# Performance work log

Measured on AMD Instinct MI355X. Metric: run time of the kernel, lower is better.

## Reference

```python
import jax, jax.numpy as jnp
import numpy as np

LN_EPS = 1e-5


def _ln(x, g, b):
    m = jnp.mean(x, axis=-1, keepdims=True)
    v = jnp.mean((x - m) ** 2, axis=-1, keepdims=True)
    return (x - m) / jnp.sqrt(v + LN_EPS) * g + b


def setup_inputs() -> dict:
    key = jax.random.key(0)
    ks = jax.random.split(key, 8)
    B, N, S, D, T = 16, 64, 2048, 1024, 768

    def xavier(k, shape):
        fan_in, fan_out = shape
        lim = (6.0 / (fan_in + fan_out)) ** 0.5
        return jax.random.uniform(k, shape, minval=-lim, maxval=lim, dtype=jnp.float32)

    return {
        "prev_states": jax.random.normal(ks[0], (B, N, D), dtype=jnp.float32),
        "input_tokens": jax.random.normal(ks[1], (B, S, T), dtype=jnp.float32),
        # input_projection (token_dim -> state_dim)
        "W_proj": xavier(ks[2], (T, D)),
        "b_proj": jnp.zeros((D,), jnp.float32),
        # three LayerNorms
        "g_state": jnp.ones((D,), jnp.float32), "beta_state": jnp.zeros((D,), jnp.float32),
        "g_input": jnp.ones((D,), jnp.float32), "beta_input": jnp.zeros((D,), jnp.float32),
        "g_out": jnp.ones((D,), jnp.float32), "beta_out": jnp.zeros((D,), jnp.float32),
        # GRU gates (2D -> D); update-gate bias initialized to -1 as in the module
        "W_u": xavier(ks[3], (2 * D, D)), "b_u": jnp.full((D,), -1.0, jnp.float32),
        "W_r": xavier(ks[4], (2 * D, D)), "b_r": jnp.zeros((D,), jnp.float32),
        "W_n": xavier(ks[5], (2 * D, D)), "b_n": jnp.zeros((D,), jnp.float32),
    }


def reference(prev_states, input_tokens, W_proj, b_proj,
              g_state, beta_state, g_input, beta_input, g_out, beta_out,
              W_u, b_u, W_r, b_r, W_n, b_n):
    D = prev_states.shape[-1]
    # project tokens to state dim: (B,S,D)
    tok = input_tokens @ W_proj + b_proj
    # attention routing (routing_weights=None path)
    scores = jnp.einsum('bnd,bsd->bns', prev_states, tok) / jnp.sqrt(jnp.float32(D))
    attn = jax.nn.softmax(scores, axis=-1)
    routed = jnp.einsum('bns,bsd->bnd', attn, tok)  # (B,N,D)
    # GRU-style gated update, vectorized over the num_states axis
    ps_n = _ln(prev_states, g_state, beta_state)
    in_n = _ln(routed, g_input, beta_input)
    concat = jnp.concatenate([ps_n, in_n], axis=-1)  # (B,N,2D)
    u = jax.nn.sigmoid(concat @ W_u + b_u)
    r = jax.nn.sigmoid(concat @ W_r + b_r)
    reset_in = jnp.concatenate([r * ps_n, in_n], axis=-1)
    cand = jnp.tanh(reset_in @ W_n + b_n)  # dropout is identity in eval
    new_state = (1.0 - u) * prev_states + u * cand
    return _ln(new_state, g_out, beta_out)
```

## Files before the change

### kernel.cpp

```cpp
#include <hip/hip_runtime.h>
#include <stdint.h>

typedef __attribute__((ext_vector_type(4))) float floatx4;
typedef __attribute__((ext_vector_type(8))) short shortx8;

#define LN_EPS 1e-5f

__device__ __forceinline__ unsigned short f2b(float f) {
  unsigned u = __builtin_bit_cast(unsigned, f);
  u = (u + 0x7FFFu + ((u >> 16) & 1u)) >> 16;
  return (unsigned short)u;
}
__device__ __forceinline__ float b2f(unsigned short h) {
  return __builtin_bit_cast(float, (unsigned)h << 16);
}

__device__ __forceinline__ void g2l16(const unsigned short* g, unsigned short* l) {
  __builtin_amdgcn_global_load_lds(
      (const __attribute__((address_space(1))) unsigned int*)g,
      (__attribute__((address_space(3))) unsigned int*)l, 16, 0, 0);
}

__device__ __forceinline__ float wave_sum(float v) {
#pragma unroll
  for (int o = 32; o; o >>= 1) v += __shfl_down(v, o, 64);
  return v;
}
__device__ __forceinline__ float block_sum(float v, float* s) {
  v = wave_sum(v);
  __syncthreads();
  if ((threadIdx.x & 63) == 0) s[threadIdx.x >> 6] = v;
  __syncthreads();
  return s[0] + s[1] + s[2] + s[3];
}

__global__ __launch_bounds__(256) void k_prep(
    const float* __restrict__ prev, unsigned short* __restrict__ psb,
    const float* __restrict__ wp, unsigned short* __restrict__ wpb,
    const float* __restrict__ Wu, const float* __restrict__ Wr,
    const float* __restrict__ Wn,
    unsigned short* __restrict__ Wtur, unsigned short* __restrict__ Wtn,
    unsigned short* __restrict__ Wtp, float* __restrict__ rs) {
  __shared__ float tile[32][33];
  const int bid = blockIdx.x;
  if (bid < 896) {
    if (bid == 0) {
      floatx4 z = {0.f, 0.f, 0.f, 0.f};
      *(floatx4*)(rs + threadIdx.x * 4) = z;
    }
    const float* src;
    unsigned short* dst;
    long i;
    if (bid < 512) { src = prev; dst = psb; i = ((long)bid * 256 + threadIdx.x) * 8; }
    else { src = wp; dst = wpb; i = ((long)(bid - 512) * 256 + threadIdx.x) * 8; }
    floatx4 v0 = *(const floatx4*)(src + i);
    floatx4 v1 = *(const floatx4*)(src + i + 4);
    unsigned short t8[8];
#pragma unroll
    for (int j = 0; j < 4; j++) { t8[j] = f2b(v0[j]); t8[4 + j] = f2b(v1[j]); }
    *(uint4*)(dst + i) = *(uint4*)t8;
    return;
  }
  int t = bid - 896;
  const float* in;
  unsigned short* out;
  int K, kx, ny;
  if (t < 6144) {
    const int which = t >> 11;
    const int t2 = t & 2047;
    kx = t2 & 63;
    ny = t2 >> 6;
    K = 2048;
    in = which == 0 ? Wu : (which == 1 ? Wr : Wn);
    out = which == 0 ? Wtur : (which == 1 ? Wtur + 1024 * 2048 : Wtn);
  } else {
    const int t2 = t - 6144;
    kx = t2 % 24;
    ny = t2 / 24;
    K = 768;
    in = wp;
    out = Wtp;
  }
  const int N = 1024;
  const int k0 = kx * 32, n0 = ny * 32;
  const int tx = threadIdx.x & 31, ty = threadIdx.x >> 5;
#pragma unroll
  for (int i = 0; i < 32; i += 8)
    tile[ty + i][tx] = in[(long)(k0 + ty + i) * N + n0 + tx];
  __syncthreads();
#pragma unroll
  for (int i = 0; i < 32; i += 8)
    out[(long)(n0 + ty + i) * K + k0 + tx] = f2b(tile[tx][ty + i]);
}

__global__ __launch_bounds__(256) void k_gemm64(
    const unsigned short* __restrict__ A, int lda,
    const unsigned short* __restrict__ Bt, int ldb,
    int K, long sCk,
    const float* __restrict__ bias, const float* __restrict__ bias2,
    int mode,
    void* __restrict__ out, int ldc,
    unsigned short* __restrict__ out2,
    const unsigned short* __restrict__ aux_psn) {
  __shared__ unsigned short As[2][64 * 64];
  __shared__ unsigned short Bs[2][64 * 64];
  const int tid = threadIdx.x;
  const int wave = tid >> 6, lane = tid & 63;
  const int kc = blockIdx.z;
  const long koff = (long)kc * K;
  const int flat = blockIdx.x + blockIdx.y * gridDim.x;
  const int q = (gridDim.x * gridDim.y) >> 3;
  const int swz = (flat & 7) * q + (flat >> 3);
  const int m0 = (swz % gridDim.x) * 64;
  const int n0 = (swz / gridDim.x) * 64;
  const int wm = wave & 1, wn = wave >> 1;
  const int l16 = lane & 15, quad = lane >> 4;
  const int srow8 = lane >> 3;
  const int c8 = ((lane & 7) ^ srow8) * 8;

  const unsigned short* gA[2];
  const unsigned short* gB[2];
  int lOff[2];
#pragma unroll
  for (int j = 0; j < 2; j++) {
    const int rb = wave * 16 + j * 8;
    gA[j] = A + (long)(m0 + rb + srow8) * lda + c8 + koff;
    gB[j] = Bt + (long)(n0 + rb + srow8) * ldb + c8 + koff;
    lOff[j] = rb * 64;
  }
  int offA[2][2], offB[2][2];
#pragma unroll
  for (int ks = 0; ks < 2; ks++)
#pragma unroll
    for (int i = 0; i < 2; i++) {
      int r = wm * 32 + i * 16 + l16;
      offA[ks][i] = r * 64 + (((ks * 4 + quad) ^ (r & 7)) * 8);
      r = wn * 32 + i * 16 + l16;
      offB[ks][i] = r * 64 + (((ks * 4 + quad) ^ (r & 7)) * 8);
    }

  floatx4 acc[2][2] = {};

#pragma unroll
  for (int j = 0; j < 2; j++) {
    g2l16(gA[j], &As[0][lOff[j]]);
    g2l16(gB[j], &Bs[0][lOff[j]]);
  }
  __syncthreads();

  const int nt = K >> 6;
  for (int t = 0; t < nt; t++) {
    const int cur = t & 1;
    if (t + 1 < nt) {
      const int kn = (t + 1) << 6;
#pragma unroll
      for (int j = 0; j < 2; j++) {
        g2l16(gA[j] + kn, &As[cur ^ 1][lOff[j]]);
        g2l16(gB[j] + kn, &Bs[cur ^ 1][lOff[j]]);
      }
    }
#pragma unroll
    for (int ks = 0; ks < 2; ks++) {
      shortx8 af[2], bf[2];
#pragma unroll
      for (int i = 0; i < 2; i++) af[i] = *(const shortx8*)&As[cur][offA[ks][i]];
#pragma unroll
      for (int j = 0; j < 2; j++) bf[j] = *(const shortx8*)&Bs[cur][offB[ks][j]];
#pragma unroll
      for (int i = 0; i < 2; i++)
#pragma unroll
        for (int j = 0; j < 2; j++)
          acc[i][j] = __builtin_amdgcn_mfma_f32_16x16x32_bf16(af[i], bf[j], acc[i][j], 0, 0, 0);
    }
    __syncthreads();
  }

#pragma unroll
  for (int i = 0; i < 2; i++)
#pragma unroll
    for (int j = 0; j < 2; j++) {
      const int rbase = m0 + wm * 32 + i * 16 + quad * 4;
      const int c = n0 + wn * 32 + j * 16 + l16;
      float bval = 0.0f;
      if (bias) bval = (mode == 5 && c >= 1024) ? bias2[c - 1024] : bias[c];
#pragma unroll
      for (int r = 0; r < 4; r++) {
        const int row = rbase + r;
        float v = acc[i][j][r] + bval;
        if (mode == 1) {
          out2[(long)row * ldc + c] = f2b(v);
        } else if (mode == 7) {
          ((float*)out)[(long)kc * sCk + (long)row * ldc + c] = v;
        } else {
          if (c < 1024) {
            ((float*)out)[(long)row * 1024 + c] = 1.0f / (1.0f + expf(-v));
          } else {
            const int cc = c - 1024;
            float rr = 1.0f / (1.0f + expf(-v));
            out2[(long)row * 2048 + cc] = f2b(rr * b2f(aux_psn[(long)row * 2048 + cc]));
          }
        }
      }
    }
}

__global__ __launch_bounds__(256) void k_gemm64_af32(
    const float* __restrict__ P0, int lda,
    const unsigned short* __restrict__ Bt, int ldb,
    int K,
    const float* __restrict__ bp, const float* __restrict__ rowsum,
    float* __restrict__ out, int ldc) {
  __shared__ unsigned short As[2][64 * 64];
  __shared__ unsigned short Bs[2][64 * 64];
  const int tid = threadIdx.x;
  const int wave = tid >> 6, lane = tid & 63;
  const int flat = blockIdx.x + blockIdx.y * gridDim.x;
  const int q = (gridDim.x * gridDim.y) >> 3;
  const int swz = (flat & 7) * q + (flat >> 3);
  const int m0 = (swz % gridDim.x) * 64;
  const int n0 = (swz / gridDim.x) * 64;
  const int wm = wave & 1, wn = wave >> 1;
  const int l16 = lane & 15, quad = lane >> 4;
  const int srow8 = lane >> 3;
  const int c8 = ((lane & 7) ^ srow8) * 8;

  const float* gAf[2];
  const unsigned short* gB[2];
  int lOff[2];
#pragma unroll
  for (int j = 0; j < 2; j++) {
    const int rb = wave * 16 + j * 8;
    gAf[j] = P0 + (long)(m0 + rb + srow8) * lda + c8;
    gB[j] = Bt + (long)(n0 + rb + srow8) * ldb + c8;
    lOff[j] = rb * 64;
  }
  int offA[2][2], offB[2][2];
#pragma unroll
  for (int ks = 0; ks < 2; ks++)
#pragma unroll
    for (int i = 0; i < 2; i++) {
      int r = wm * 32 + i * 16 + l16;
      offA[ks][i] = r * 64 + (((ks * 4 + quad) ^ (r & 7)) * 8);
      r = wn * 32 + i * 16 + l16;
      offB[ks][i] = r * 64 + (((ks * 4 + quad) ^ (r & 7)) * 8);
    }

  floatx4 acc[2][2] = {};

#pragma unroll
  for (int j = 0; j < 2; j++) {
    g2l16(gB[j], &Bs[0][lOff[j]]);
    floatx4 a0 = *(const floatx4*)(gAf[j]);
    floatx4 a1 = *(const floatx4*)(gAf[j] + 4);
    floatx4 b0 = *(const floatx4*)(gAf[j] + 786432);
    floatx4 b1 = *(const floatx4*)(gAf[j] + 786432 + 4);
    unsigned short t8[8];
#pragma unroll
    for (int i = 0; i < 4; i++) { t8[i] = f2b(a0[i] + b0[i]); t8[4 + i] = f2b(a1[i] + b1[i]); }
    *(uint4*)&As[0][lOff[j] + lane * 8] = *(uint4*)t8;
  }
  __syncthreads();

  const int nt = K >> 6;
  for (int t = 0; t < nt; t++) {
    const int cur = t & 1;
    floatx4 a0[2], a1[2], p0[2], p1[2];
    if (t + 1 < nt) {
      const int kn = (t + 1) << 6;
#pragma unroll
      for (int j = 0; j < 2; j++) {
        g2l16(gB[j] + kn, &Bs[cur ^ 1][lOff[j]]);
        a0[j] = *(const floatx4*)(gAf[j] + kn);
        a1[j] = *(const floatx4*)(gAf[j] + kn + 4);
        p0[j] = *(const floatx4*)(gAf[j] + kn + 786432);
        p1[j] = *(const floatx4*)(gAf[j] + kn + 786432 + 4);
      }
    }
#pragma unroll
    for (int ks = 0; ks < 2; ks++) {
      shortx8 af[2], bf[2];
#pragma unroll
      for (int i = 0; i < 2; i++) af[i] = *(const shortx8*)&As[cur][offA[ks][i]];
#pragma unroll
      for (int j = 0; j < 2; j++) bf[j] = *(const shortx8*)&Bs[cur][offB[ks][j]];
#pragma unroll
      for (int i = 0; i < 2; i++)
#pragma unroll
        for (int j = 0; j < 2; j++)
          acc[i][j] = __builtin_amdgcn_mfma_f32_16x16x32_bf16(af[i], bf[j], acc[i][j], 0, 0, 0);
    }
    if (t + 1 < nt) {
#pragma unroll
      for (int j = 0; j < 2; j++) {
        unsigned short t8[8];
#pragma unroll
        for (int i = 0; i < 4; i++) {
          t8[i] = f2b(a0[j][i] + p0[j][i]);
          t8[4 + i] = f2b(a1[j][i] + p1[j][i]);
        }
        *(uint4*)&As[cur ^ 1][lOff[j] + lane * 8] = *(uint4*)t8;
      }
    }
    __syncthreads();
  }

#pragma unroll
  for (int i = 0; i < 2; i++)
#pragma unroll
    for (int j = 0; j < 2; j++) {
      const int rbase = m0 + wm * 32 + i * 16 + quad * 4;
      const int c = n0 + wn * 32 + j * 16 + l16;
#pragma unroll
      for (int r = 0; r < 4; r++) {
        const int row = rbase + r;
        out[(long)row * ldc + c] = acc[i][j][r] + rowsum[row] * bp[c];
      }
    }
}

__global__ __launch_bounds__(256) void k_scores(
    const unsigned short* __restrict__ A, long sAb, int lda,
    const float* __restrict__ toksf,
    int K, float scale,
    unsigned short* __restrict__ out2, int ldc, long sCb,
    float* __restrict__ rs) {
  __shared__ unsigned short As[2][64 * 64];
  __shared__ unsigned short Bs[2][64 * 64];
  const int tid = threadIdx.x;
  const int wave = tid >> 6, lane = tid & 63;
  const int b = blockIdx.z;
  const int m0 = 0, n0 = blockIdx.y * 64;
  const int wm = wave & 1, wn = wave >> 1;
  const int l16 = lane & 15, quad = lane >> 4;
  const int srow8 = lane >> 3;
  const int c8 = ((lane & 7) ^ srow8) * 8;
  const unsigned short* Ab = A + (long)b * sAb;

  const unsigned short* gA[2];
  const float* gBf[2];
  int lOff[2];
#pragma unroll
  for (int j = 0; j < 2; j++) {
    const int rb = wave * 16 + j * 8;
    gA[j] = Ab + (long)(m0 + rb + srow8) * lda + c8;
    gBf[j] = toksf + (long)b * 1572864 + (long)(n0 + rb + srow8) * 768 + c8;
    lOff[j] = rb * 64;
  }
  int offA[2][2], offB[2][2];
#pragma unroll
  for (int ks = 0; ks < 2; ks++)
#pragma unroll
    for (int i = 0; i < 2; i++) {
      int r = wm * 32 + i * 16 + l16;
      offA[ks][i] = r * 64 + (((ks * 4 + quad) ^ (r & 7)) * 8);
      r = wn * 32 + i * 16 + l16;
      offB[ks][i] = r * 64 + (((ks * 4 + quad) ^ (r & 7)) * 8);
    }

  floatx4 acc[2][2] = {};

#pragma unroll
  for (int j = 0; j < 2; j++) {
    g2l16(gA[j], &As[0][lOff[j]]);
    floatx4 v0 = *(const floatx4*)(gBf[j]);
    floatx4 v1 = *(const floatx4*)(gBf[j] + 4);
    unsigned short t8[8];
#pragma unroll
    for (int i = 0; i < 4; i++) { t8[i] = f2b(v0[i]); t8[4 + i] = f2b(v1[i]); }
    *(uint4*)&Bs[0][lOff[j] + lane * 8] = *(uint4*)t8;
  }
  __syncthreads();

  const int nt = K >> 6;
  for (int t = 0; t < nt; t++) {
    const int cur = t & 1;
    floatx4 w0[2], w1[2];
    if (t + 1 < nt) {
      const int kn = (t + 1) << 6;
#pragma unroll
      for (int j = 0; j < 2; j++) {
        g2l16(gA[j] + kn, &As[cur ^ 1][lOff[j]]);
        w0[j] = *(const floatx4*)(gBf[j] + kn);
        w1[j] = *(const floatx4*)(gBf[j] + kn + 4);
      }
    }
#pragma unroll
    for (int ks = 0; ks < 2; ks++) {
      shortx8 af[2], bf[2];
#pragma unroll
      for (int i = 0; i < 2; i++) af[i] = *(const shortx8*)&As[cur][offA[ks][i]];
#pragma unroll
      for (int j = 0; j < 2; j++) bf[j] = *(const shortx8*)&Bs[cur][offB[ks][j]];
#pragma unroll
      for (int i = 0; i < 2; i++)
#pragma unroll
        for (int j = 0; j < 2; j++)
          acc[i][j] = __builtin_amdgcn_mfma_f32_16x16x32_bf16(af[i], bf[j], acc[i][j], 0, 0, 0);
    }
    if (t + 1 < nt) {
#pragma unroll
      for (int j = 0; j < 2; j++) {
        unsigned short t8[8];
#pragma unroll
        for (int i = 0; i < 4; i++) { t8[i] = f2b(w0[j][i]); t8[4 + i] = f2b(w1[j][i]); }
        *(uint4*)&Bs[cur ^ 1][lOff[j] + lane * 8] = *(uint4*)t8;
      }
    }
    __syncthreads();
  }

#pragma unroll
  for (int i = 0; i < 2; i++) {
    float psum[4] = {0.f, 0.f, 0.f, 0.f};
#pragma unroll
    for (int j = 0; j < 2; j++) {
      const int rbase = m0 + wm * 32 + i * 16 + quad * 4;
      const int c = n0 + wn * 32 + j * 16 + l16;
#pragma unroll
      for (int r = 0; r < 4; r++) {
        const float e = expf(acc[i][j][r] * scale);
        out2[(long)b * sCb + (long)(rbase + r) * ldc + c] = f2b(e);
        psum[r] += e;
      }
    }
#pragma unroll
    for (int r = 0; r < 4; r++) {
      float s = psum[r];
      s += __shfl_xor(s, 1, 64);
      s += __shfl_xor(s, 2, 64);
      s += __shfl_xor(s, 4, 64);
      s += __shfl_xor(s, 8, 64);
      if (l16 == 0)
        atomicAdd(rs + (long)b * 64 + m0 + wm * 32 + i * 16 + quad * 4 + r, s);
    }
  }
}

__global__ __launch_bounds__(256) void k_routed_mfma(
    const unsigned short* __restrict__ attnb,
    const float* __restrict__ tokf,
    float* __restrict__ parts) {
  __shared__ unsigned short As[64 * 40];
  __shared__ unsigned short Bs[32 * 66];
  const int kc = blockIdx.x, nt = blockIdx.y, b = blockIdx.z;
  const int tid = threadIdx.x;
  const int wave = tid >> 6, lane = tid & 63;
  const int wm = wave & 1, wn = wave >> 1;
  const int l16 = lane & 15, quad = lane >> 4;
  const int n0 = nt * 64;
  const long abase = (long)b * 131072 + (long)kc * 1024;
  const long tbase = ((long)b * 2048 + (long)kc * 1024) * 768;
  const int srow = tid >> 2, skc = (tid & 3) * 8;
  const int bk = tid >> 3, bd = (tid & 7) * 8;

  floatx4 acc[2][2] = {};

  uint4 pa = *(const uint4*)(attnb + abase + (long)srow * 2048 + skc);
  floatx4 f0 = *(const floatx4*)(tokf + tbase + (long)bk * 768 + n0 + bd);
  floatx4 f1 = *(const floatx4*)(tokf + tbase + (long)bk * 768 + n0 + bd + 4);

  for (int k0 = 0; k0 < 1024; k0 += 32) {
    *(uint4*)&As[srow * 40 + skc] = pa;
    {
      unsigned short t8[8];
#pragma unroll
      for (int i = 0; i < 4; i++) { t8[i] = f2b(f0[i]); t8[4 + i] = f2b(f1[i]); }
      unsigned short* dst = &Bs[bk * 66 + bd];
#pragma unroll
      for (int w2 = 0; w2 < 4; w2++) *(unsigned*)(dst + w2 * 2) = ((unsigned*)t8)[w2];
    }
    if (k0 + 32 < 1024) {
      pa = *(const uint4*)(attnb + abase + (long)srow * 2048 + (k0 + 32) + skc);
      f0 = *(const floatx4*)(tokf + tbase + (long)(k0 + 32 + bk) * 768 + n0 + bd);
      f1 = *(const floatx4*)(tokf + tbase + (long)(k0 + 32 + bk) * 768 + n0 + bd + 4);
    }
    asm volatile("s_waitcnt lgkmcnt(0)" ::: "memory");
    __builtin_amdgcn_s_barrier();
    __builtin_amdgcn_sched_barrier(0);

    shortx8 a0 = *(const shortx8*)&As[(wm * 32 + 0  + l16) * 40 + quad * 8];
    shortx8 a1 = *(const shortx8*)&As[(wm * 32 + 16 + l16) * 40 + quad * 8];
    shortx8 b0, b1;
#pragma unroll
    for (int j = 0; j < 8; j++) {
      b0[j] = *(const short*)&Bs[(quad * 8 + j) * 66 + wn * 32 + l16];
      b1[j] = *(const short*)&Bs[(quad * 8 + j) * 66 + wn * 32 + 16 + l16];
    }
    acc[0][0] = __builtin_amdgcn_mfma_f32_16x16x32_bf16(a0, b0, acc[0][0], 0, 0, 0);
    acc[0][1] = __builtin_amdgcn_mfma_f32_16x16x32_bf16(a0, b1, acc[0][1], 0, 0, 0);
    acc[1][0] = __builtin_amdgcn_mfma_f32_16x16x32_bf16(a1, b0, acc[1][0], 0, 0, 0);
    acc[1][1] = __builtin_amdgcn_mfma_f32_16x16x32_bf16(a1, b1, acc[1][1], 0, 0, 0);
    __builtin_amdgcn_s_barrier();
  }

#pragma unroll
  for (int im = 0; im < 2; im++)
#pragma unroll
    for (int in_ = 0; in_ < 2; in_++) {
      const int rbase = wm * 32 + im * 16 + quad * 4;
      const int c = n0 + wn * 32 + in_ * 16 + l16;
#pragma unroll
      for (int r = 0; r < 4; r++)
        parts[(long)kc * 786432 + ((long)b * 64 + rbase + r) * 768 + c] =
            acc[im][in_][r];
    }
}

__global__ __launch_bounds__(256) void k_ln2(
    const float* __restrict__ prev, const float* __restrict__ routed,
    const float* __restrict__ g_st, const float* __restrict__ be_st,
    const float* __restrict__ g_in, const float* __restrict__ be_in,
    unsigned short* __restrict__ conc, unsigned short* __restrict__ candA) {
  __shared__ float scr[4];
  const long r = blockIdx.x & 1023;
  const bool second = blockIdx.x >= 1024;
  const int t = threadIdx.x;
  floatx4 v;
  const float *g, *be;
  if (!second) {
    v = *(const floatx4*)(prev + r * 1024 + t * 4);
    g = g_st; be = be_st;
  } else {
    v = *(const floatx4*)(routed + r * 1024 + t * 4);
    g = g_in; be = be_in;
  }
  float s1 = v[0] + v[1] + v[2] + v[3];
  float s2 = v[0] * v[0] + v[1] * v[1] + v[2] * v[2] + v[3] * v[3];
  s1 = block_sum(s1, scr);
  s2 = block_sum(s2, scr);
  const float mean = s1 * (1.0f / 1024.0f);
  const float var = s2 * (1.0f / 1024.0f) - mean * mean;
  const float rstd = rsqrtf(var + LN_EPS);
#pragma unroll
  for (int i = 0; i < 4; i++) {
    const int d = t * 4 + i;
    const float y = (v[i] - mean) * rstd * g[d] + be[d];
    const unsigned short h = f2b(y);
    if (!second) {
      conc[r * 2048 + d] = h;
    } else {
      conc[r * 2048 + 1024 + d] = h;
      candA[r * 2048 + 1024 + d] = h;
    }
  }
}

__global__ __launch_bounds__(256) void k_gate_epi(
    const float* __restrict__ gparts,
    const float* __restrict__ bu, const float* __restrict__ br,
    const unsigned short* __restrict__ conc,
    float* __restrict__ ubuf, unsigned short* __restrict__ candA) {
  const int row = blockIdx.x >> 1;
  const int half = blockIdx.x & 1;
  const int t = threadIdx.x;
  const long base = (long)row * 2048 + half * 1024 + t * 4;
  floatx4 p0 = *(const floatx4*)(gparts + base);
  floatx4 p1 = *(const floatx4*)(gparts + 2097152 + base);
  const float* bias = half ? br : bu;
  floatx4 bv = *(const floatx4*)(bias + t * 4);
  if (!half) {
    floatx4 o;
#pragma unroll
    for (int i = 0; i < 4; i++)
      o[i] = 1.0f / (1.0f + expf(-(p0[i] + p1[i] + bv[i])));
    *(floatx4*)(ubuf + (long)row * 1024 + t * 4) = o;
  } else {
    unsigned short t4[4];
#pragma unroll
    for (int i = 0; i < 4; i++) {
      float rr = 1.0f / (1.0f + expf(-(p0[i] + p1[i] + bv[i])));
      t4[i] = f2b(rr * b2f(conc[(long)row * 2048 + t * 4 + i]));
    }
    *(uint2*)(candA + (long)row * 2048 + t * 4) = *(uint2*)t4;
  }
}

__global__ __launch_bounds__(256) void k_ln_out(
    const float* __restrict__ cparts,
    const float* __restrict__ ubuf, const float* __restrict__ prev,
    const float* __restrict__ bn,
    const float* __restrict__ g, const float* __restrict__ be,
    float* __restrict__ out) {
  __shared__ float scr[4];
  const long r = blockIdx.x;
  const int t = threadIdx.x;
  floatx4 p0 = *(const floatx4*)(cparts + r * 1024 + t * 4);
  floatx4 p1 = *(const floatx4*)(cparts + 1048576 + r * 1024 + t * 4);
  floatx4 uu = *(const floatx4*)(ubuf + r * 1024 + t * 4);
  floatx4 pv = *(const floatx4*)(prev + r * 1024 + t * 4);
  floatx4 bv = *(const floatx4*)(bn + t * 4);
  floatx4 v;
#pragma unroll
  for (int i = 0; i < 4; i++) {
    const float cand = tanhf(p0[i] + p1[i] + bv[i]);
    v[i] = (1.0f - uu[i]) * pv[i] + uu[i] * cand;
  }
  float s1 = v[0] + v[1] + v[2] + v[3];
  float s2 = v[0] * v[0] + v[1] * v[1] + v[2] * v[2] + v[3] * v[3];
  s1 = block_sum(s1, scr);
  s2 = block_sum(s2, scr);
  const float mean = s1 * (1.0f / 1024.0f);
  const float var = s2 * (1.0f / 1024.0f) - mean * mean;
  const float rstd = rsqrtf(var + LN_EPS);
  floatx4 o;
#pragma unroll
  for (int i = 0; i < 4; i++) {
    const int d = t * 4 + i;
    o[i] = (v[i] - mean) * rstd * g[d] + be[d];
  }
  *(floatx4*)(out + r * 1024 + t * 4) = o;
}

extern "C" void kernel_launch(void* const* d_in, const int* in_sizes, int n_in,
                              void* d_out, int out_size, void* d_ws, size_t ws_size,
                              hipStream_t stream) {
  (void)in_sizes; (void)n_in; (void)out_size; (void)ws_size;
  const float* prev  = (const float*)d_in[0];
  const float* toks  = (const float*)d_in[1];
  const float* Wp    = (const float*)d_in[2];
  const float* bp    = (const float*)d_in[3];
  const float* g_st  = (const float*)d_in[4];
  const float* be_st = (const float*)d_in[5];
  const float* g_in  = (const float*)d_in[6];
  const float* be_in = (const float*)d_in[7];
  const float* g_o   = (const float*)d_in[8];
  const float* be_o  = (const float*)d_in[9];
  const float* Wu    = (const float*)d_in[10];
  const float* bu    = (const float*)d_in[11];
  const float* Wr    = (const float*)d_in[12];
  const float* br    = (const float*)d_in[13];
  const float* Wn    = (const float*)d_in[14];
  const float* bn    = (const float*)d_in[15];
  float* out = (float*)d_out;

  char* ws = (char*)d_ws;
  unsigned short* psb   = (unsigned short*)ws; ws += 2097152;
  unsigned short* Wpb   = (unsigned short*)ws; ws += 1572864;
  unsigned short* Wtp   = (unsigned short*)ws; ws += 1572864;
  unsigned short* pwb   = (unsigned short*)ws; ws += 1572864;
  unsigned short* attnb = (unsigned short*)ws; ws += 4194304;
  float*          rowsum= (float*)ws;          ws += 4096;
  float*          parts = (float*)ws;          ws += 6291456;
  float*          routed= (float*)ws;          ws += 4194304;
  unsigned short* conc  = (unsigned short*)ws; ws += 4194304;
  unsigned short* candA = (unsigned short*)ws; ws += 4194304;
  float*          ubuf  = (float*)ws;          ws += 4194304;
  unsigned short* Wtur  = (unsigned short*)ws; ws += 8388608;
  unsigned short* Wtn   = (unsigned short*)ws; ws += 4194304;
  float*          gparts= (float*)ws;          ws += 16777216;
  float*          cparts= (float*)ws;          ws += 8388608;

  const dim3 blk(256);

  k_prep<<<dim3(7808), blk, 0, stream>>>(prev, psb, Wp, Wpb,
                                         Wu, Wr, Wn, Wtur, Wtn, Wtp, rowsum);
  k_gemm64<<<dim3(16, 12, 1), blk, 0, stream>>>(
      psb, 1024, Wpb, 1024, 1024, 0L,
      nullptr, nullptr, 1,
      nullptr, 768, pwb, nullptr);
  k_scores<<<dim3(1, 32, 16), blk, 0, stream>>>(
      pwb, 49152L, 768, toks, 768, 0.03125f,
      attnb, 2048, 131072L, rowsum);
  k_routed_mfma<<<dim3(2, 12, 16), blk, 0, stream>>>(attnb, toks, parts);
  k_gemm64_af32<<<dim3(16, 16), blk, 0, stream>>>(
      parts, 768, Wtp, 768, 768, bp, rowsum, routed, 1024);
  k_ln2<<<dim3(2048), blk, 0, stream>>>(prev, routed, g_st, be_st, g_in, be_in,
                                        conc, candA);
  k_gemm64<<<dim3(16, 32, 2), blk, 0, stream>>>(
      conc, 2048, Wtur, 2048, 1024, 2097152L,
      nullptr, nullptr, 7,
      (void*)gparts, 2048, nullptr, nullptr);
  k_gate_epi<<<dim3(2048), blk, 0, stream>>>(gparts, bu, br, conc, ubuf, candA);
  k_gemm64<<<dim3(16, 16, 2), blk, 0, stream>>>(
      candA, 2048, Wtn, 2048, 1024, 1048576L,
      nullptr, nullptr, 7,
      (void*)cparts, 1024, nullptr, nullptr);
  k_ln_out<<<dim3(1024), blk, 0, stream>>>(cparts, ubuf, prev, bn, g_o, be_o, out);
}
```

Baseline: 305.5 us.

## Fuse fp32-to-bf16 conversion into prev×Wp GEMM inside prep kernel; fold state LN into proj GEMM

```diff
diff --git a/kernel.cpp b/kernel.cpp
--- a/kernel.cpp
+++ b/kernel.cpp
@@ -34,34 +34,128 @@
   return s[0] + s[1] + s[2] + s[3];
 }
 
-__global__ __launch_bounds__(256) void k_prep(
-    const float* __restrict__ prev, unsigned short* __restrict__ psb,
-    const float* __restrict__ wp, unsigned short* __restrict__ wpb,
+__global__ __launch_bounds__(256) void k_prep_pw(
+    const float* __restrict__ prev, const float* __restrict__ wp,
     const float* __restrict__ Wu, const float* __restrict__ Wr,
     const float* __restrict__ Wn,
     unsigned short* __restrict__ Wtur, unsigned short* __restrict__ Wtn,
-    unsigned short* __restrict__ Wtp, float* __restrict__ rs) {
-  __shared__ float tile[32][33];
+    unsigned short* __restrict__ Wtp, unsigned short* __restrict__ pwb,
+    float* __restrict__ rs) {
+  __shared__ unsigned short As[2][64 * 64];
+  __shared__ unsigned short Bs[2][64 * 64];
   const int bid = blockIdx.x;
-  if (bid < 896) {
-    if (bid == 0) {
-      floatx4 z = {0.f, 0.f, 0.f, 0.f};
-      *(floatx4*)(rs + threadIdx.x * 4) = z;
-    }
-    const float* src;
-    unsigned short* dst;
-    long i;
-    if (bid < 512) { src = prev; dst = psb; i = ((long)bid * 256 + threadIdx.x) * 8; }
-    else { src = wp; dst = wpb; i = ((long)(bid - 512) * 256 + threadIdx.x) * 8; }
-    floatx4 v0 = *(const floatx4*)(src + i);
-    floatx4 v1 = *(const floatx4*)(src + i + 4);
-    unsigned short t8[8];
-#pragma unroll
-    for (int j = 0; j < 4; j++) { t8[j] = f2b(v0[j]); t8[4 + j] = f2b(v1[j]); }
-    *(uint4*)(dst + i) = *(uint4*)t8;
+  const int tid = threadIdx.x;
+  if (bid < 192) {
+    const int wave = tid >> 6, lane = tid & 63;
+    const int swz = (bid & 7) * 24 + (bid >> 3);
+    const int m0 = (swz % 16) * 64;
+    const int n0 = (swz / 16) * 64;
+    const int wm = wave & 1, wn = wave >> 1;
+    const int l16 = lane & 15, quad = lane >> 4;
+    const int srow8 = lane >> 3;
+    const int c8 = ((lane & 7) ^ srow8) * 8;
+
+    const float* gAf[2];
+    const float* gBf[2];
+    int lOff[2];
+#pragma unroll
+    for (int j = 0; j < 2; j++) {
+      const int rb = wave * 16 + j * 8;
+      gAf[j] = prev + (long)(m0 + rb + srow8) * 1024 + c8;
+      gBf[j] = wp + (long)(n0 + rb + srow8) * 1024 + c8;
+      lOff[j] = rb * 64;
+    }
+    int offA[2][2], offB[2][2];
+#pragma unroll
+    for (int ks = 0; ks < 2; ks++)
+#pragma unroll
+      for (int i = 0; i < 2; i++) {
+        int r = wm * 32 + i * 16 + l16;
+        offA[ks][i] = r * 64 + (((ks * 4 + quad) ^ (r & 7)) * 8);
+        r = wn * 32 + i * 16 + l16;
+        offB[ks][i] = r * 64 + (((ks * 4 + quad) ^ (r & 7)) * 8);
+      }
+
+    floatx4 acc[2][2] = {};
+
+#pragma unroll
+    for (int j = 0; j < 2; j++) {
+      floatx4 a0 = *(const floatx4*)(gAf[j]);
+      floatx4 a1 = *(const floatx4*)(gAf[j] + 4);
+      floatx4 b0 = *(const floatx4*)(gBf[j]);
+      floatx4 b1 = *(const floatx4*)(gBf[j] + 4);
+      unsigned short ta[8], tb[8];
+#pragma unroll
+      for (int i = 0; i < 4; i++) {
+        ta[i] = f2b(a0[i]); ta[4 + i] = f2b(a1[i]);
+        tb[i] = f2b(b0[i]); tb[4 + i] = f2b(b1[i]);
+      }
+      *(uint4*)&As[0][lOff[j] + lane * 8] = *(uint4*)ta;
+      *(uint4*)&Bs[0][lOff[j] + lane * 8] = *(uint4*)tb;
+    }
+    __syncthreads();
+
+    const int nt = 16;
+    for (int t = 0; t < nt; t++) {
+      const int cur = t & 1;
+      floatx4 a0[2], a1[2], b0[2], b1[2];
+      if (t + 1 < nt) {
+        const int kn = (t + 1) << 6;
+#pragma unroll
+        for (int j = 0; j < 2; j++) {
+          a0[j] = *(const floatx4*)(gAf[j] + kn);
+          a1[j] = *(const floatx4*)(gAf[j] + kn + 4);
+          b0[j] = *(const floatx4*)(gBf[j] + kn);
+          b1[j] = *(const floatx4*)(gBf[j] + kn + 4);
+        }
+      }
+#pragma unroll
+      for (int ks = 0; ks < 2; ks++) {
+        shortx8 af[2], bf[2];
+#pragma unroll
+        for (int i = 0; i < 2; i++) af[i] = *(const shortx8*)&As[cur][offA[ks][i]];
+#pragma unroll
+        for (int j = 0; j < 2; j++) bf[j] = *(const shortx8*)&Bs[cur][offB[ks][j]];
+#pragma unroll
+        for (int i = 0; i < 2; i++)
+#pragma unroll
+          for (int j = 0; j < 2; j++)
+            acc[i][j] = __builtin_amdgcn_mfma_f32_16x16x32_bf16(af[i], bf[j], acc[i][j], 0, 0, 0);
+      }
+      if (t + 1 < nt) {
+#pragma unroll
+        for (int j = 0; j < 2; j++) {
+          unsigned short ta[8], tb[8];
+#pragma unroll
+          for (int i = 0; i < 4; i++) {
+            ta[i] = f2b(a0[j][i]); ta[4 + i] = f2b(a1[j][i]);
+            tb[i] = f2b(b0[j][i]); tb[4 + i] = f2b(b1[j][i]);
+          }
+          *(uint4*)&As[cur ^ 1][lOff[j] + lane * 8] = *(uint4*)ta;
+          *(uint4*)&Bs[cur ^ 1][lOff[j] + lane * 8] = *(uint4*)tb;
+        }
+      }
+      __syncthreads();
+    }
+
+#pragma unroll
+    for (int i = 0; i < 2; i++)
+#pragma unroll
+      for (int j = 0; j < 2; j++) {
+        const int rbase = m0 + wm * 32 + i * 16 + quad * 4;
+        const int c = n0 + wn * 32 + j * 16 + l16;
+#pragma unroll
+        for (int r = 0; r < 4; r++)
+          pwb[(long)(rbase + r) * 768 + c] = f2b(acc[i][j][r]);
+      }
     return;
   }
-  int t = bid - 896;
+  float(*tile)[33] = (float(*)[33]) & As[0][0];
+  if (bid == 192) {
+    floatx4 z = {0.f, 0.f, 0.f, 0.f};
+    *(floatx4*)(rs + tid * 4) = z;
+  }
+  int t = bid - 192;
   const float* in;
   unsigned short* out;
   int K, kx, ny;
@@ -83,7 +177,7 @@
   }
   const int N = 1024;
   const int k0 = kx * 32, n0 = ny * 32;
-  const int tx = threadIdx.x & 31, ty = threadIdx.x >> 5;
+  const int tx = tid & 31, ty = tid >> 5;
 #pragma unroll
   for (int i = 0; i < 32; i += 8)
     tile[ty + i][tx] = in[(long)(k0 + ty + i) * N + n0 + tx];
@@ -97,11 +191,7 @@
     const unsigned short* __restrict__ A, int lda,
     const unsigned short* __restrict__ Bt, int ldb,
     int K, long sCk,
-    const float* __restrict__ bias, const float* __restrict__ bias2,
-    int mode,
-    void* __restrict__ out, int ldc,
-    unsigned short* __restrict__ out2,
-    const unsigned short* __restrict__ aux_psn) {
+    float* __restrict__ out, int ldc) {
   __shared__ unsigned short As[2][64 * 64];
   __shared__ unsigned short Bs[2][64 * 64];
   const int tid = threadIdx.x;
@@ -181,44 +271,49 @@
     for (int j = 0; j < 2; j++) {
       const int rbase = m0 + wm * 32 + i * 16 + quad * 4;
       const int c = n0 + wn * 32 + j * 16 + l16;
-      float bval = 0.0f;
-      if (bias) bval = (mode == 5 && c >= 1024) ? bias2[c - 1024] : bias[c];
-#pragma unroll
-      for (int r = 0; r < 4; r++) {
-        const int row = rbase + r;
-        float v = acc[i][j][r] + bval;
-        if (mode == 1) {
-          out2[(long)row * ldc + c] = f2b(v);
-        } else if (mode == 7) {
-          ((float*)out)[(long)kc * sCk + (long)row * ldc + c] = v;
-        } else {
-          if (c < 1024) {
-            ((float*)out)[(long)row * 1024 + c] = 1.0f / (1.0f + expf(-v));
-          } else {
-            const int cc = c - 1024;
-            float rr = 1.0f / (1.0f + expf(-v));
-            out2[(long)row * 2048 + cc] = f2b(rr * b2f(aux_psn[(long)row * 2048 + cc]));
-          }
-        }
-      }
-    }
-}
-
-__global__ __launch_bounds__(256) void k_gemm64_af32(
+#pragma unroll
+      for (int r = 0; r < 4; r++)
+        out[(long)kc * sCk + (long)(rbase + r) * ldc + c] = acc[i][j][r];
+    }
+}
+
+__global__ __launch_bounds__(256) void k_proj2_ln(
     const float* __restrict__ P0, int lda,
     const unsigned short* __restrict__ Bt, int ldb,
     int K,
     const float* __restrict__ bp, const float* __restrict__ rowsum,
-    float* __restrict__ out, int ldc) {
+    float* __restrict__ out, int ldc,
+    const float* __restrict__ prev,
+    const float* __restrict__ g_st, const float* __restrict__ be_st,
+    unsigned short* __restrict__ conc) {
   __shared__ unsigned short As[2][64 * 64];
   __shared__ unsigned short Bs[2][64 * 64];
   const int tid = threadIdx.x;
+  if (blockIdx.x >= 256) {
+    float* scr = (float*)&As[0][0];
+    const long r = blockIdx.x - 256;
+    floatx4 v = *(const floatx4*)(prev + r * 1024 + tid * 4);
+    float s1 = v[0] + v[1] + v[2] + v[3];
+    float s2 = v[0] * v[0] + v[1] * v[1] + v[2] * v[2] + v[3] * v[3];
+    s1 = block_sum(s1, scr);
+    s2 = block_sum(s2, scr);
+    const float mean = s1 * (1.0f / 1024.0f);
+    const float var = s2 * (1.0f / 1024.0f) - mean * mean;
+    const float rstd = rsqrtf(var + LN_EPS);
+    unsigned short t4[4];
+#pragma unroll
+    for (int i = 0; i < 4; i++) {
+      const int d = tid * 4 + i;
+      t4[i] = f2b((v[i] - mean) * rstd * g_st[d] + be_st[d]);
+    }
+    *(uint2*)(conc + r * 2048 + tid * 4) = *(uint2*)t4;
+    return;
+  }
   const int wave = tid >> 6, lane = tid & 63;
-  const int flat = blockIdx.x + blockIdx.y * gridDim.x;
-  const int q = (gridDim.x * gridDim.y) >> 3;
-  const int swz = (flat & 7) * q + (flat >> 3);
-  const int m0 = (swz % gridDim.x) * 64;
-  const int n0 = (swz / gridDim.x) * 64;
+  const int flat = blockIdx.x;
+  const int swz = (flat & 7) * 32 + (flat >> 3);
+  const int m0 = (swz % 16) * 64;
+  const int n0 = (swz / 16) * 64;
   const int wm = wave & 1, wn = wave >> 1;
   const int l16 = lane & 15, quad = lane >> 4;
   const int srow8 = lane >> 3;
@@ -506,24 +601,14 @@
     }
 }
 
-__global__ __launch_bounds__(256) void k_ln2(
-    const float* __restrict__ prev, const float* __restrict__ routed,
-    const float* __restrict__ g_st, const float* __restrict__ be_st,
+__global__ __launch_bounds__(256) void k_ln_routed(
+    const float* __restrict__ routed,
     const float* __restrict__ g_in, const float* __restrict__ be_in,
     unsigned short* __restrict__ conc, unsigned short* __restrict__ candA) {
   __shared__ float scr[4];
-  const long r = blockIdx.x & 1023;
-  const bool second = blockIdx.x >= 1024;
+  const long r = blockIdx.x;
   const int t = threadIdx.x;
-  floatx4 v;
-  const float *g, *be;
-  if (!second) {
-    v = *(const floatx4*)(prev + r * 1024 + t * 4);
-    g = g_st; be = be_st;
-  } else {
-    v = *(const floatx4*)(routed + r * 1024 + t * 4);
-    g = g_in; be = be_in;
-  }
+  floatx4 v = *(const floatx4*)(routed + r * 1024 + t * 4);
   float s1 = v[0] + v[1] + v[2] + v[3];
   float s2 = v[0] * v[0] + v[1] * v[1] + v[2] * v[2] + v[3] * v[3];
   s1 = block_sum(s1, scr);
@@ -531,18 +616,14 @@
   const float mean = s1 * (1.0f / 1024.0f);
   const float var = s2 * (1.0f / 1024.0f) - mean * mean;
   const float rstd = rsqrtf(var + LN_EPS);
+  unsigned short t4[4];
 #pragma unroll
   for (int i = 0; i < 4; i++) {
     const int d = t * 4 + i;
-    const float y = (v[i] - mean) * rstd * g[d] + be[d];
-    const unsigned short h = f2b(y);
-    if (!second) {
-      conc[r * 2048 + d] = h;
-    } else {
-      conc[r * 2048 + 1024 + d] = h;
-      candA[r * 2048 + 1024 + d] = h;
-    }
-  }
+    t4[i] = f2b((v[i] - mean) * rstd * g_in[d] + be_in[d]);
+  }
+  *(uint2*)(conc + r * 2048 + 1024 + t * 4) = *(uint2*)t4;
+  *(uint2*)(candA + r * 2048 + 1024 + t * 4) = *(uint2*)t4;
 }
 
 __global__ __launch_bounds__(256) void k_gate_epi(
@@ -634,8 +715,6 @@
   float* out = (float*)d_out;
 
   char* ws = (char*)d_ws;
-  unsigned short* psb   = (unsigned short*)ws; ws += 2097152;
-  unsigned short* Wpb   = (unsigned short*)ws; ws += 1572864;
   unsigned short* Wtp   = (unsigned short*)ws; ws += 1572864;
   unsigned short* pwb   = (unsigned short*)ws; ws += 1572864;
   unsigned short* attnb = (unsigned short*)ws; ws += 4194304;
@@ -652,28 +731,20 @@
 
   const dim3 blk(256);
 
-  k_prep<<<dim3(7808), blk, 0, stream>>>(prev, psb, Wp, Wpb,
-                                         Wu, Wr, Wn, Wtur, Wtn, Wtp, rowsum);
-  k_gemm64<<<dim3(16, 12, 1), blk, 0, stream>>>(
-      psb, 1024, Wpb, 1024, 1024, 0L,
-      nullptr, nullptr, 1,
-      nullptr, 768, pwb, nullptr);
+  k_prep_pw<<<dim3(7104), blk, 0, stream>>>(prev, Wp, Wu, Wr, Wn,
+                                            Wtur, Wtn, Wtp, pwb, rowsum);
   k_scores<<<dim3(1, 32, 16), blk, 0, stream>>>(
       pwb, 49152L, 768, toks, 768, 0.03125f,
       attnb, 2048, 131072L, rowsum);
   k_routed_mfma<<<dim3(2, 12, 16), blk, 0, stream>>>(attnb, toks, parts);
-  k_gemm64_af32<<<dim3(16, 16), blk, 0, stream>>>(
-      parts, 768, Wtp, 768, 768, bp, rowsum, routed, 1024);
-  k_ln2<<<dim3(2048), blk, 0, stream>>>(prev, routed, g_st, be_st, g_in, be_in,
-                                        conc, candA);
+  k_proj2_ln<<<dim3(1280), blk, 0, stream>>>(
+      parts, 768, Wtp, 768, 768, bp, rowsum, routed, 1024,
+      prev, g_st, be_st, conc);
+  k_ln_routed<<<dim3(1024), blk, 0, stream>>>(routed, g_in, be_in, conc, candA);
   k_gemm64<<<dim3(16, 32, 2), blk, 0, stream>>>(
-      conc, 2048, Wtur, 2048, 1024, 2097152L,
-      nullptr, nullptr, 7,
-      (void*)gparts, 2048, nullptr, nullptr);
+      conc, 2048, Wtur, 2048, 1024, 2097152L, gparts, 2048);
   k_gate_epi<<<dim3(2048), blk, 0, stream>>>(gparts, bu, br, conc, ubuf, candA);
   k_gemm64<<<dim3(16, 16, 2), blk, 0, stream>>>(
-      candA, 2048, Wtn, 2048, 1024, 1048576L,
-      nullptr, nullptr, 7,
-      (void*)cparts, 1024, nullptr, nullptr);
+      candA, 2048, Wtn, 2048, 1024, 1048576L, cparts, 1024);
   k_ln_out<<<dim3(1024), blk, 0, stream>>>(cparts, ubuf, prev, bn, g_o, be_o, out);
 }
```

Result: faster. 294.8 us, median of 2 (-3.5%).
